# Performance work log

Hardware: AMD Instinct MI355X
Metric: run time of the kernel (lower is better)

The kernel has to match this reference:

```python
import jax, jax.numpy as jnp
from jax import lax
import numpy as np

EPS = 1e-3  # keras BatchNormalization epsilon
ALPHA = 0.3  # LeakyReLU slope


def setup_inputs() -> dict:
    key = jax.random.key(0)
    ks = jax.random.split(key, 7)
    B, H, W, C = 16, 64, 64, 1024
    G, Cg = 32, C // 32
    x = jax.random.normal(ks[0], (B, H, W, C), dtype=jnp.float32)
    # depthwise kernel, HWIO with feature_group_count=C (depth_multiplier=1)
    dw_kernel = jax.random.normal(ks[1], (3, 3, 1, C), dtype=jnp.float32) * 0.1
    # block-diagonal pointwise: per-group [Cg_in, Cg_out]
    pw_kernel = jax.random.normal(ks[2], (G, Cg, Cg), dtype=jnp.float32) * 0.1
    gamma = jax.random.uniform(ks[3], (C,), dtype=jnp.float32, minval=0.5, maxval=1.5)
    beta = jax.random.normal(ks[4], (C,), dtype=jnp.float32) * 0.1
    moving_mean = jax.random.normal(ks[5], (C,), dtype=jnp.float32) * 0.1
    moving_var = jax.random.uniform(ks[6], (C,), dtype=jnp.float32, minval=0.5, maxval=1.5)
    return {"x": x, "dw_kernel": dw_kernel, "pw_kernel": pw_kernel,
            "gamma": gamma, "beta": beta,
            "moving_mean": moving_mean, "moving_var": moving_var}


def reference(x, dw_kernel, pw_kernel, gamma, beta, moving_mean, moving_var):
    B, H, W, C = x.shape
    G, Cg, _ = pw_kernel.shape
    # depthwise 3x3, 'same' padding, one filter per channel -> all groups at once
    y = lax.conv_general_dilated(
        x, dw_kernel, window_strides=(1, 1), padding='SAME',
        dimension_numbers=('NHWC', 'HWIO', 'NHWC'), feature_group_count=C)
    # block-diagonal pointwise conv (per-group Cg->Cg 1x1)
    y = y.reshape(B, H, W, G, Cg)
    y = jnp.einsum('bhwgc,gcd->bhwgd', y, pw_kernel).reshape(B, H, W, C)
    # inference BatchNorm (per-group BNs concatenated == per-channel over C)
    scale = gamma * lax.rsqrt(moving_var + EPS)
    y = y * scale + (beta - moving_mean * scale)
    # LeakyReLU(alpha=0.3)
    return jnp.where(y >= 0, y, ALPHA * y)
```

## Files before the change

kernel.cpp:

```cpp
#include <hip/hip_runtime.h>

#define BATCH 16
#define HH 64
#define WW 64
#define CC 1024
#define GG 32
#define CG 32
#define TH 8
#define TW 16
#define EPS 1e-3f
#define ALPHA 0.3f

#define XS_FLOATS ((TH + 2) * (TW + 2) * CG)
#define YS_STRIDE 36

__global__ __launch_bounds__(256, 4)
void fused_dw_pw_bn_lrelu(const float* __restrict__ x,
                          const float* __restrict__ dwk,
                          const float* __restrict__ pwk,
                          const float* __restrict__ gamma,
                          const float* __restrict__ beta,
                          const float* __restrict__ mmean,
                          const float* __restrict__ mvar,
                          float* __restrict__ out) {
    __shared__ float smem[XS_FLOATS];

    const int t = threadIdx.x;
    const int tilesW = WW / TW;
    const int tile  = blockIdx.x;
    const int tw0   = (tile % tilesW) * TW;
    const int th0   = (tile / tilesW) * TH;
    const int g     = blockIdx.y;
    const int b     = blockIdx.z;
    const int cbase = g * CG;

    for (int i = t; i < (TH + 2) * (TW + 2) * 8; i += 256) {
        int q   = i & 7;
        int pp  = i >> 3;
        int r   = pp / (TW + 2);
        int col = pp % (TW + 2);
        int gh  = th0 - 1 + r;
        int gw  = tw0 - 1 + col;
        float4 v = make_float4(0.f, 0.f, 0.f, 0.f);
        if (gh >= 0 && gh < HH && gw >= 0 && gw < WW) {
            v = *(const float4*)(x + ((size_t)(b * HH + gh) * WW + gw) * CC + cbase + q * 4);
        }
        *(float4*)(smem + (size_t)pp * CG + q * 4) = v;
    }

    const int c4    = (t & 7) * 4;
    const int pslot = t >> 3;
    float4 k9[9];
    #pragma unroll
    for (int j = 0; j < 9; ++j)
        k9[j] = *(const float4*)(dwk + j * CC + cbase + c4);

    __syncthreads();

    float4 yv[4];
    #pragma unroll
    for (int i = 0; i < 4; ++i) {
        int p  = pslot + i * 32;
        int pr = p / TW, pc = p % TW;
        float4 acc = make_float4(0.f, 0.f, 0.f, 0.f);
        #pragma unroll
        for (int dy = 0; dy < 3; ++dy) {
            #pragma unroll
            for (int dx = 0; dx < 3; ++dx) {
                float4 xv = *(const float4*)(smem + ((pr + dy) * (TW + 2) + (pc + dx)) * CG + c4);
                float4 kk = k9[dy * 3 + dx];
                acc.x += xv.x * kk.x;
                acc.y += xv.y * kk.y;
                acc.z += xv.z * kk.z;
                acc.w += xv.w * kk.w;
            }
        }
        yv[i] = acc;
    }

    __syncthreads();

    #pragma unroll
    for (int i = 0; i < 4; ++i) {
        int p = pslot + i * 32;
        *(float4*)(smem + p * YS_STRIDE + c4) = yv[i];
    }

    const int d   = t & (CG - 1);
    const int ps2 = t >> 5;
    float wreg[CG];
    #pragma unroll
    for (int c = 0; c < CG; ++c)
        wreg[c] = pwk[(g * CG + c) * CG + d];
    float sc = gamma[cbase + d] * rsqrtf(mvar[cbase + d] + EPS);
    float bi = beta[cbase + d] - mmean[cbase + d] * sc;

    __syncthreads();

    for (int i = 0; i < 16; ++i) {
        int p = ps2 + i * 8;
        float acc = 0.f;
        #pragma unroll
        for (int cq = 0; cq < 8; ++cq) {
            float4 y4 = *(const float4*)(smem + p * YS_STRIDE + cq * 4);
            acc += y4.x * wreg[cq * 4 + 0] + y4.y * wreg[cq * 4 + 1]
                 + y4.z * wreg[cq * 4 + 2] + y4.w * wreg[cq * 4 + 3];
        }
        float z = acc * sc + bi;
        z = (z >= 0.f) ? z : ALPHA * z;
        int pr = p / TW, pc = p % TW;
        out[((size_t)(b * HH + (th0 + pr)) * WW + (tw0 + pc)) * CC + cbase + d] = z;
    }
}

extern "C" void kernel_launch(void* const* d_in, const int* in_sizes, int n_in,
                              void* d_out, int out_size, void* d_ws, size_t ws_size,
                              hipStream_t stream) {
    const float* x     = (const float*)d_in[0];
    const float* dwk   = (const float*)d_in[1];
    const float* pwk   = (const float*)d_in[2];
    const float* gamma = (const float*)d_in[3];
    const float* beta  = (const float*)d_in[4];
    const float* mmean = (const float*)d_in[5];
    const float* mvar  = (const float*)d_in[6];
    float* out = (float*)d_out;

    dim3 grid((HH / TH) * (WW / TW), GG, BATCH);
    dim3 block(256);
    hipLaunchKernelGGL(fused_dw_pw_bn_lrelu, grid, block, 0, stream,
                       x, dwk, pwk, gamma, beta, mmean, mvar, out);
}
```

Measured before the change: 507.1 us.

## Register-block depthwise rows and pointwise outputs with float4 stores

The depthwise stage now has each thread compute four vertically adjacent pixels. Each loaded input row of three float4s is reused across up to three output rows, which cuts shared-memory reads from 36 to 18 float4s per thread. The pointwise stage gives each thread 4 output channels for 4 pixels, loading weights as float4 from global, and writes results with float4 stores instead of scalar stores. This reduces LDS traffic and store instruction count, at the cost of higher register pressure under the existing launch bounds.

```diff
diff --git a/kernel.cpp b/kernel.cpp
--- a/kernel.cpp
+++ b/kernel.cpp
@@ -50,6 +50,8 @@
 
     const int c4    = (t & 7) * 4;
     const int pslot = t >> 3;
+    const int pcol  = pslot & 15;
+    const int pr0   = (pslot >> 4) * 4;
     float4 k9[9];
     #pragma unroll
     for (int j = 0; j < 9; ++j)
@@ -57,59 +59,86 @@
 
     __syncthreads();
 
-    float4 yv[4];
+    float4 acc[4];
     #pragma unroll
-    for (int i = 0; i < 4; ++i) {
-        int p  = pslot + i * 32;
-        int pr = p / TW, pc = p % TW;
-        float4 acc = make_float4(0.f, 0.f, 0.f, 0.f);
+    for (int i = 0; i < 4; ++i) acc[i] = make_float4(0.f, 0.f, 0.f, 0.f);
+
+    #pragma unroll
+    for (int xr = 0; xr < 6; ++xr) {
+        float4 xq[3];
         #pragma unroll
-        for (int dy = 0; dy < 3; ++dy) {
-            #pragma unroll
-            for (int dx = 0; dx < 3; ++dx) {
-                float4 xv = *(const float4*)(smem + ((pr + dy) * (TW + 2) + (pc + dx)) * CG + c4);
-                float4 kk = k9[dy * 3 + dx];
-                acc.x += xv.x * kk.x;
-                acc.y += xv.y * kk.y;
-                acc.z += xv.z * kk.z;
-                acc.w += xv.w * kk.w;
+        for (int dx = 0; dx < 3; ++dx)
+            xq[dx] = *(const float4*)(smem + ((pr0 + xr) * (TW + 2) + (pcol + dx)) * CG + c4);
+        #pragma unroll
+        for (int i = 0; i < 4; ++i) {
+            const int dy = xr - i;
+            if (dy >= 0 && dy <= 2) {
+                #pragma unroll
+                for (int dx = 0; dx < 3; ++dx) {
+                    float4 kk = k9[dy * 3 + dx];
+                    acc[i].x += xq[dx].x * kk.x;
+                    acc[i].y += xq[dx].y * kk.y;
+                    acc[i].z += xq[dx].z * kk.z;
+                    acc[i].w += xq[dx].w * kk.w;
+                }
             }
         }
-        yv[i] = acc;
     }
 
     __syncthreads();
 
     #pragma unroll
     for (int i = 0; i < 4; ++i) {
-        int p = pslot + i * 32;
-        *(float4*)(smem + p * YS_STRIDE + c4) = yv[i];
+        int p = (pr0 + i) * TW + pcol;
+        *(float4*)(smem + p * YS_STRIDE + c4) = acc[i];
     }
 
-    const int d   = t & (CG - 1);
-    const int ps2 = t >> 5;
-    float wreg[CG];
-    #pragma unroll
-    for (int c = 0; c < CG; ++c)
-        wreg[c] = pwk[(g * CG + c) * CG + d];
-    float sc = gamma[cbase + d] * rsqrtf(mvar[cbase + d] + EPS);
-    float bi = beta[cbase + d] - mmean[cbase + d] * sc;
+    const int d4  = (t & 7) * 4;
+    const int ps2 = t >> 3;
+    float4 gm = *(const float4*)(gamma + cbase + d4);
+    float4 bt = *(const float4*)(beta  + cbase + d4);
+    float4 mm = *(const float4*)(mmean + cbase + d4);
+    float4 mv = *(const float4*)(mvar  + cbase + d4);
+    float4 sc, bi;
+    sc.x = gm.x * rsqrtf(mv.x + EPS);  bi.x = bt.x - mm.x * sc.x;
+    sc.y = gm.y * rsqrtf(mv.y + EPS);  bi.y = bt.y - mm.y * sc.y;
+    sc.z = gm.z * rsqrtf(mv.z + EPS);  bi.z = bt.z - mm.z * sc.z;
+    sc.w = gm.w * rsqrtf(mv.w + EPS);  bi.w = bt.w - mm.w * sc.w;
 
     __syncthreads();
 
-    for (int i = 0; i < 16; ++i) {
-        int p = ps2 + i * 8;
-        float acc = 0.f;
+    float4 o[4];
+    #pragma unroll
+    for (int i = 0; i < 4; ++i) o[i] = make_float4(0.f, 0.f, 0.f, 0.f);
+
+    const float* wg = pwk + (size_t)g * CG * CG;
+    #pragma unroll
+    for (int cq = 0; cq < 8; ++cq) {
+        float4 w0 = *(const float4*)(wg + (cq * 4 + 0) * CG + d4);
+        float4 w1 = *(const float4*)(wg + (cq * 4 + 1) * CG + d4);
+        float4 w2 = *(const float4*)(wg + (cq * 4 + 2) * CG + d4);
+        float4 w3 = *(const float4*)(wg + (cq * 4 + 3) * CG + d4);
         #pragma unroll
-        for (int cq = 0; cq < 8; ++cq) {
+        for (int i = 0; i < 4; ++i) {
+            int p = ps2 + i * 32;
             float4 y4 = *(const float4*)(smem + p * YS_STRIDE + cq * 4);
-            acc += y4.x * wreg[cq * 4 + 0] + y4.y * wreg[cq * 4 + 1]
-                 + y4.z * wreg[cq * 4 + 2] + y4.w * wreg[cq * 4 + 3];
+            o[i].x += y4.x * w0.x + y4.y * w1.x + y4.z * w2.x + y4.w * w3.x;
+            o[i].y += y4.x * w0.y + y4.y * w1.y + y4.z * w2.y + y4.w * w3.y;
+            o[i].z += y4.x * w0.z + y4.y * w1.z + y4.z * w2.z + y4.w * w3.z;
+            o[i].w += y4.x * w0.w + y4.y * w1.w + y4.z * w2.w + y4.w * w3.w;
         }
-        float z = acc * sc + bi;
-        z = (z >= 0.f) ? z : ALPHA * z;
-        int pr = p / TW, pc = p % TW;
-        out[((size_t)(b * HH + (th0 + pr)) * WW + (tw0 + pc)) * CC + cbase + d] = z;
+    }
+
+    #pragma unroll
+    for (int i = 0; i < 4; ++i) {
+        int p  = ps2 + i * 32;
+        int pr = p >> 4, pc = p & 15;
+        float4 z;
+        z.x = o[i].x * sc.x + bi.x;  z.x = (z.x >= 0.f) ? z.x : ALPHA * z.x;
+        z.y = o[i].y * sc.y + bi.y;  z.y = (z.y >= 0.f) ? z.y : ALPHA * z.y;
+        z.z = o[i].z * sc.z + bi.z;  z.z = (z.z >= 0.f) ? z.z : ALPHA * z.z;
+        z.w = o[i].w * sc.w + bi.w;  z.w = (z.w >= 0.f) ? z.w : ALPHA * z.w;
+        *(float4*)(out + ((size_t)(b * HH + (th0 + pr)) * WW + (tw0 + pc)) * CC + cbase + d4) = z;
     }
 }
 
```

Result: slower. 963.9 us (+90.1%).

## Compute depthwise conv from global loads with register row sliding, vectorize pointwise

Applied to the files above, without the earlier changes.

The depthwise stage no longer stages the haloed input tile in shared memory. Each thread now owns one column and two channels and walks down the tile rows, loading three neighbouring pixels per row from global memory and accumulating into eight row accumulators. Boundaries are handled with clamped offsets and multiplicative masks. The pointwise stage now computes 8 output channels times 2 pixels per thread using packed float2 FMAs and float4 weight loads, and writes float4 stores. This drops a shared-memory load phase and a barrier, and shrinks the shared footprint. In exchange, horizontal halo reuse now depends on the L1/L2 cache, and the global loads are narrower (8 bytes instead of 16).

```diff
diff --git a/kernel.cpp b/kernel.cpp
--- a/kernel.cpp
+++ b/kernel.cpp
@@ -11,8 +11,33 @@
 #define EPS 1e-3f
 #define ALPHA 0.3f
 
-#define XS_FLOATS ((TH + 2) * (TW + 2) * CG)
+typedef float v2f __attribute__((ext_vector_type(2)));
+
 #define YS_STRIDE 36
+#define YS_FLOATS (TH * TW * YS_STRIDE)
+
+#define ROWLD \
+    v2f x0 = *(const v2f*)(rrp + o0) * cm0; \
+    v2f x1 = *(const v2f*)(rrp + o1); \
+    v2f x2 = *(const v2f*)(rrp + o2) * cm2;
+
+#define ROW3(AA, BB, CC_) { \
+    ROWLD \
+    AA  += x0 * k0 + x1 * k1 + x2 * k2; \
+    BB  += x0 * k3 + x1 * k4 + x2 * k5; \
+    CC_ += x0 * k6 + x1 * k7 + x2 * k8; \
+    rrp += WW * CC; }
+
+#define PWSTEP(J, YA, YB) { \
+    const float* wj = wcp + (J) * CG; \
+    float4 wA = *(const float4*)(wj); \
+    float4 wB = *(const float4*)(wj + 4); \
+    v2f wv0 = {wA.x, wA.y}, wv1 = {wA.z, wA.w}; \
+    v2f wv2 = {wB.x, wB.y}, wv3 = {wB.z, wB.w}; \
+    p0a += wv0 * (YA); p1a += wv1 * (YA); p2a += wv2 * (YA); p3a += wv3 * (YA); \
+    p0b += wv0 * (YB); p1b += wv1 * (YB); p2b += wv2 * (YB); p3b += wv3 * (YB); }
+
+#define LR(v) ((v) >= 0.f ? (v) : ALPHA * (v))
 
 __global__ __launch_bounds__(256, 4)
 void fused_dw_pw_bn_lrelu(const float* __restrict__ x,
@@ -23,93 +48,131 @@
                           const float* __restrict__ mmean,
                           const float* __restrict__ mvar,
                           float* __restrict__ out) {
-    __shared__ float smem[XS_FLOATS];
+    __shared__ float smem[YS_FLOATS];
 
-    const int t = threadIdx.x;
-    const int tilesW = WW / TW;
+    const int t     = threadIdx.x;
     const int tile  = blockIdx.x;
-    const int tw0   = (tile % tilesW) * TW;
-    const int th0   = (tile / tilesW) * TH;
+    const int tw0   = (tile & 3) * TW;
+    const int th0   = (tile >> 2) * TH;
     const int g     = blockIdx.y;
     const int b     = blockIdx.z;
     const int cbase = g * CG;
 
-    for (int i = t; i < (TH + 2) * (TW + 2) * 8; i += 256) {
-        int q   = i & 7;
-        int pp  = i >> 3;
-        int r   = pp / (TW + 2);
-        int col = pp % (TW + 2);
-        int gh  = th0 - 1 + r;
-        int gw  = tw0 - 1 + col;
-        float4 v = make_float4(0.f, 0.f, 0.f, 0.f);
-        if (gh >= 0 && gh < HH && gw >= 0 && gw < WW) {
-            v = *(const float4*)(x + ((size_t)(b * HH + gh) * WW + gw) * CC + cbase + q * 4);
-        }
-        *(float4*)(smem + (size_t)pp * CG + q * 4) = v;
+    const int c2i  = t & 15;
+    const int c2   = c2i * 2;
+    const int pcol = t >> 4;
+
+    const float* kp = dwk + cbase + c2;
+    v2f k0 = *(const v2f*)(kp + 0 * CC), k1 = *(const v2f*)(kp + 1 * CC), k2 = *(const v2f*)(kp + 2 * CC);
+    v2f k3 = *(const v2f*)(kp + 3 * CC), k4 = *(const v2f*)(kp + 4 * CC), k5 = *(const v2f*)(kp + 5 * CC);
+    v2f k6 = *(const v2f*)(kp + 6 * CC), k7 = *(const v2f*)(kp + 7 * CC), k8 = *(const v2f*)(kp + 8 * CC);
+
+    const int gw0 = tw0 + pcol - 1;
+    const int gw2 = gw0 + 2;
+    const float cm0 = (gw0 >= 0) ? 1.f : 0.f;
+    const float cm2 = (gw2 < WW) ? 1.f : 0.f;
+    const int o0 = ((gw0 < 0) ? 0 : gw0) * CC;
+    const int o1 = (gw0 + 1) * CC;
+    const int o2 = ((gw2 >= WW) ? (WW - 1) : gw2) * CC;
+
+    const float* rrp = x + ((size_t)(b * HH + th0) * WW) * CC + cbase + c2;
+
+    v2f a0 = {0.f, 0.f};
+    v2f a1 = a0, a2 = a0, a3 = a0, a4 = a0, a5 = a0, a6 = a0, a7 = a0;
+
+    if (th0 > 0) {
+        const float* q = rrp - WW * CC;
+        v2f x0 = *(const v2f*)(q + o0) * cm0;
+        v2f x1 = *(const v2f*)(q + o1);
+        v2f x2 = *(const v2f*)(q + o2) * cm2;
+        a0 += x0 * k0 + x1 * k1 + x2 * k2;
+    }
+    {
+        ROWLD
+        a1 += x0 * k0 + x1 * k1 + x2 * k2;
+        a0 += x0 * k3 + x1 * k4 + x2 * k5;
+        rrp += WW * CC;
+    }
+    ROW3(a2, a1, a0)
+    ROW3(a3, a2, a1)
+    ROW3(a4, a3, a2)
+    ROW3(a5, a4, a3)
+    ROW3(a6, a5, a4)
+    ROW3(a7, a6, a5)
+    {
+        ROWLD
+        a7 += x0 * k3 + x1 * k4 + x2 * k5;
+        a6 += x0 * k6 + x1 * k7 + x2 * k8;
+        rrp += WW * CC;
+    }
+    if (th0 < HH - TH) {
+        ROWLD
+        a7 += x0 * k6 + x1 * k7 + x2 * k8;
     }
 
-    const int c4    = (t & 7) * 4;
-    const int pslot = t >> 3;
-    float4 k9[9];
-    #pragma unroll
-    for (int j = 0; j < 9; ++j)
-        k9[j] = *(const float4*)(dwk + j * CC + cbase + c4);
-
-    __syncthreads();
-
-    float4 yv[4];
-    #pragma unroll
-    for (int i = 0; i < 4; ++i) {
-        int p  = pslot + i * 32;
-        int pr = p / TW, pc = p % TW;
-        float4 acc = make_float4(0.f, 0.f, 0.f, 0.f);
-        #pragma unroll
-        for (int dy = 0; dy < 3; ++dy) {
-            #pragma unroll
-            for (int dx = 0; dx < 3; ++dx) {
-                float4 xv = *(const float4*)(smem + ((pr + dy) * (TW + 2) + (pc + dx)) * CG + c4);
-                float4 kk = k9[dy * 3 + dx];
-                acc.x += xv.x * kk.x;
-                acc.y += xv.y * kk.y;
-                acc.z += xv.z * kk.z;
-                acc.w += xv.w * kk.w;
-            }
-        }
-        yv[i] = acc;
+    {
+        float* ys = smem + pcol * YS_STRIDE + c2;
+        *(v2f*)(ys + 0 * TW * YS_STRIDE) = a0;
+        *(v2f*)(ys + 1 * TW * YS_STRIDE) = a1;
+        *(v2f*)(ys + 2 * TW * YS_STRIDE) = a2;
+        *(v2f*)(ys + 3 * TW * YS_STRIDE) = a3;
+        *(v2f*)(ys + 4 * TW * YS_STRIDE) = a4;
+        *(v2f*)(ys + 5 * TW * YS_STRIDE) = a5;
+        *(v2f*)(ys + 6 * TW * YS_STRIDE) = a6;
+        *(v2f*)(ys + 7 * TW * YS_STRIDE) = a7;
     }
 
     __syncthreads();
 
+    const int d8  = (t & 3) * 8;
+    const int px0 = t >> 2;
+    const float* wg = pwk + (size_t)g * CG * CG + d8;
+
+    v2f p0a = {0.f, 0.f}, p1a = p0a, p2a = p0a, p3a = p0a;
+    v2f p0b = p0a, p1b = p0a, p2b = p0a, p3b = p0a;
+
     #pragma unroll
-    for (int i = 0; i < 4; ++i) {
-        int p = pslot + i * 32;
-        *(float4*)(smem + p * YS_STRIDE + c4) = yv[i];
+    for (int cq = 0; cq < 8; ++cq) {
+        const float* wcp = wg + cq * 4 * CG;
+        float4 ya = *(const float4*)(smem + px0 * YS_STRIDE + cq * 4);
+        float4 yb = *(const float4*)(smem + px0 * YS_STRIDE + 64 * YS_STRIDE + cq * 4);
+        PWSTEP(0, ya.x, yb.x)
+        PWSTEP(1, ya.y, yb.y)
+        PWSTEP(2, ya.z, yb.z)
+        PWSTEP(3, ya.w, yb.w)
     }
 
-    const int d   = t & (CG - 1);
-    const int ps2 = t >> 5;
-    float wreg[CG];
-    #pragma unroll
-    for (int c = 0; c < CG; ++c)
-        wreg[c] = pwk[(g * CG + c) * CG + d];
-    float sc = gamma[cbase + d] * rsqrtf(mvar[cbase + d] + EPS);
-    float bi = beta[cbase + d] - mmean[cbase + d] * sc;
+    float4 gA = *(const float4*)(gamma + cbase + d8), gB = *(const float4*)(gamma + cbase + d8 + 4);
+    float4 vA = *(const float4*)(mvar  + cbase + d8), vB = *(const float4*)(mvar  + cbase + d8 + 4);
+    float4 bA = *(const float4*)(beta  + cbase + d8), bB = *(const float4*)(beta  + cbase + d8 + 4);
+    float4 mA = *(const float4*)(mmean + cbase + d8), mB = *(const float4*)(mmean + cbase + d8 + 4);
+    float s0 = gA.x * rsqrtf(vA.x + EPS), s1 = gA.y * rsqrtf(vA.y + EPS);
+    float s2 = gA.z * rsqrtf(vA.z + EPS), s3 = gA.w * rsqrtf(vA.w + EPS);
+    float s4 = gB.x * rsqrtf(vB.x + EPS), s5 = gB.y * rsqrtf(vB.y + EPS);
+    float s6 = gB.z * rsqrtf(vB.z + EPS), s7 = gB.w * rsqrtf(vB.w + EPS);
+    float c0 = bA.x - mA.x * s0, c1 = bA.y - mA.y * s1;
+    float c2b = bA.z - mA.z * s2, c3 = bA.w - mA.w * s3;
+    float c4 = bB.x - mB.x * s4, c5 = bB.y - mB.y * s5;
+    float c6 = bB.z - mB.z * s6, c7 = bB.w - mB.w * s7;
 
-    __syncthreads();
-
-    for (int i = 0; i < 16; ++i) {
-        int p = ps2 + i * 8;
-        float acc = 0.f;
-        #pragma unroll
-        for (int cq = 0; cq < 8; ++cq) {
-            float4 y4 = *(const float4*)(smem + p * YS_STRIDE + cq * 4);
-            acc += y4.x * wreg[cq * 4 + 0] + y4.y * wreg[cq * 4 + 1]
-                 + y4.z * wreg[cq * 4 + 2] + y4.w * wreg[cq * 4 + 3];
-        }
-        float z = acc * sc + bi;
-        z = (z >= 0.f) ? z : ALPHA * z;
-        int pr = p / TW, pc = p % TW;
-        out[((size_t)(b * HH + (th0 + pr)) * WW + (tw0 + pc)) * CC + cbase + d] = z;
+    const int pr = px0 >> 4, pc = px0 & 15;
+    float* op = out + ((size_t)(b * HH + th0 + pr) * WW + (tw0 + pc)) * CC + cbase + d8;
+    {
+        float z0 = LR(p0a.x * s0 + c0),  z1 = LR(p0a.y * s1 + c1);
+        float z2 = LR(p1a.x * s2 + c2b), z3 = LR(p1a.y * s3 + c3);
+        float z4 = LR(p2a.x * s4 + c4),  z5 = LR(p2a.y * s5 + c5);
+        float z6 = LR(p3a.x * s6 + c6),  z7 = LR(p3a.y * s7 + c7);
+        *(float4*)(op)     = make_float4(z0, z1, z2, z3);
+        *(float4*)(op + 4) = make_float4(z4, z5, z6, z7);
+    }
+    {
+        float* op2 = op + (size_t)4 * WW * CC;
+        float z0 = LR(p0b.x * s0 + c0),  z1 = LR(p0b.y * s1 + c1);
+        float z2 = LR(p1b.x * s2 + c2b), z3 = LR(p1b.y * s3 + c3);
+        float z4 = LR(p2b.x * s4 + c4),  z5 = LR(p2b.y * s5 + c5);
+        float z6 = LR(p3b.x * s6 + c6),  z7 = LR(p3b.y * s7 + c7);
+        *(float4*)(op2)     = make_float4(z0, z1, z2, z3);
+        *(float4*)(op2 + 4) = make_float4(z4, z5, z6, z7);
     }
 }
 
```

Result: slower. 645.2 us (+27.2%).
